# Kernel tuning notes

Hardware: AMD Instinct MI355X
Metric: run time of the kernel (lower is better)

## Reference

```python
import jax, jax.numpy as jnp
import numpy as np

N = 10000       # nodes
E = 640000      # edges
D_IN = 128
D_OUT = 128
EPS = 1e-5      # LayerNorm eps (torch default)


def setup_inputs() -> dict:
    key = jax.random.key(0)
    k_x, k_e, k_w, k_b, k_g = jax.random.split(key, 5)
    x = jax.random.normal(k_x, (N, D_IN), dtype=jnp.float32)
    edge_index = jax.random.randint(k_e, (2, E), 0, N, dtype=jnp.int64)
    # GCNConv linear weight (PyG uses glorot) and bias
    lim = float(np.sqrt(6.0 / (D_IN + D_OUT)))
    W = jax.random.uniform(k_w, (D_IN, D_OUT), minval=-lim, maxval=lim, dtype=jnp.float32)
    b = jnp.zeros((D_OUT,), dtype=jnp.float32)
    # LayerNorm affine params
    gamma = jnp.ones((D_OUT,), dtype=jnp.float32)
    beta = jnp.zeros((D_OUT,), dtype=jnp.float32)
    return {"x": x, "edge_index": edge_index, "W": W, "b": b, "gamma": gamma, "beta": beta}


def reference(x, edge_index, W, b, gamma, beta):
    # --- GCNConv: A_hat = D^{-1/2} (A + I) D^{-1/2}; out = A_hat X W + b ---
    self_idx = jnp.arange(N, dtype=edge_index.dtype)
    src = jnp.concatenate([edge_index[0], self_idx])  # [E+N]
    dst = jnp.concatenate([edge_index[1], self_idx])  # [E+N]
    deg = jax.ops.segment_sum(jnp.ones_like(src, dtype=x.dtype), dst, num_segments=N)
    dinv = jnp.where(deg > 0, jax.lax.rsqrt(deg), 0.0)  # [N]
    norm = dinv[src] * dinv[dst]                        # [E+N]
    h = x @ W                                           # [N, D_OUT] transform first (cheaper)
    msg = h[src] * norm[:, None]                        # [E+N, D_OUT]
    out = jax.ops.segment_sum(msg, dst, num_segments=N) + b
    # --- LayerNorm over feature dim ---
    mu = jnp.mean(out, axis=-1, keepdims=True)
    var = jnp.mean(jnp.square(out - mu), axis=-1, keepdims=True)
    out = (out - mu) * jax.lax.rsqrt(var + EPS) * gamma + beta
    # act = Identity (last_act=ReLU is truthy -> Identity branch); dropout = eval identity; residual=False
    return out
```

## Files before the change

### kernel.cpp

```cpp
#include <hip/hip_runtime.h>
#include <hip/hip_fp16.h>

#define D 128
#define LN_EPS 1e-5f


static __device__ __forceinline__ float h2f(unsigned short h) {
    return __half2float(__builtin_bit_cast(__half, h));
}
static __device__ __forceinline__ unsigned short f2h(float f) {
    return __builtin_bit_cast(unsigned short, __float2half_rn(f));
}

static __device__ __forceinline__ void flagbar(int* slots, int c, int C, int phase) {
    __syncthreads();
    int val = 0x5A5A0001 + phase;
    int tid = threadIdx.x;
    if (tid == 0)
        __hip_atomic_store(&slots[phase * 64 + c], val, __ATOMIC_RELEASE, __HIP_MEMORY_SCOPE_AGENT);
    if (tid < C) {
        while (__hip_atomic_load(&slots[phase * 64 + tid], __ATOMIC_ACQUIRE, __HIP_MEMORY_SCOPE_AGENT) != val)
            __builtin_amdgcn_s_sleep(1);
    }
    __syncthreads();
}

__global__ __launch_bounds__(1024) void build_kernel(
        const int* __restrict__ src, const int* __restrict__ dst,
        const float* __restrict__ W, unsigned int* __restrict__ Wh,
        unsigned short* __restrict__ ghist, int* __restrict__ blocksum,
        int* __restrict__ rowptr, float* __restrict__ dinv,
        unsigned short* __restrict__ csr, int* __restrict__ bar,
        int N, int E, int Ec, int NW, int C) {
    extern __shared__ int lds[];
    __shared__ int s_scan[20];
    int c = blockIdx.x;
    int tid = threadIdx.x;
    int lane = tid & 63, wv = tid >> 6;

    for (int i = tid; i < N; i += 1024) lds[i] = 0;
    int gs = gridDim.x * 1024;
    for (int i = c * 1024 + tid; i < NW; i += gs) {
        float2 v = ((const float2*)W)[i];
        Wh[i] = (unsigned int)f2h(v.x) | ((unsigned int)f2h(v.y) << 16);
    }
    __syncthreads();
    int lo = c * Ec, hi = min(lo + Ec, E);
    #pragma unroll 4
    for (int i = lo + tid; i < hi; i += 1024)
        atomicAdd(&lds[dst[i]], 1);
    __syncthreads();
    for (int i = tid; i < N; i += 1024)
        ghist[(size_t)c * N + i] = (unsigned short)lds[i];
    flagbar(bar, c, C, 0);

    int nper = (N + C - 1) / C;
    int n0 = c * nper;
    int nn = min(nper, N - n0); if (nn < 0) nn = 0;
    int mydeg = 0;
    if (tid < nn) {
        int n = n0 + tid;
        int run = 0;
        #pragma unroll 8
        for (int cc = 0; cc < C; cc++) {
            int t = ghist[(size_t)cc * N + n];
            ghist[(size_t)cc * N + n] = (unsigned short)run;
            run += t;
        }
        mydeg = run;
        dinv[n] = rsqrtf((float)(run + 1));
    }
    int incl = mydeg;
    #pragma unroll
    for (int off = 1; off < 64; off <<= 1) {
        int y = __shfl_up(incl, off);
        if (lane >= off) incl += y;
    }
    if (lane == 63) s_scan[wv] = incl;
    __syncthreads();
    if (tid == 0) {
        int run = 0;
        #pragma unroll
        for (int k = 0; k < 16; k++) { int t = s_scan[k]; s_scan[k] = run; run += t; }
        blocksum[c] = run;
    }
    __syncthreads();
    if (tid < nn) rowptr[n0 + tid] = s_scan[wv] + incl - mydeg;
    flagbar(bar, c, C, 1);

    if (tid < 64) {
        int bs = (tid < C) ? blocksum[tid] : 0;
        int inc2 = bs;
        #pragma unroll
        for (int off = 1; off < 64; off <<= 1) {
            int y = __shfl_up(inc2, off);
            if (tid >= off) inc2 += y;
        }
        if (tid == c)     s_scan[18] = inc2 - bs;
        if (tid == C - 1) s_scan[19] = inc2;
    }
    __syncthreads();
    int base = s_scan[18];
    if (tid < nn) rowptr[n0 + tid] += base;
    if (c == C - 1 && tid == 0) rowptr[N] = s_scan[19];
    flagbar(bar, c, C, 2);

    for (int i = tid; i < N; i += 1024)
        lds[i] = rowptr[i] + ghist[(size_t)c * N + i];
    __syncthreads();
    #pragma unroll 4
    for (int i = lo + tid; i < hi; i += 1024) {
        int d = dst[i];
        int pos = atomicAdd(&lds[d], 1);
        csr[pos] = (unsigned short)src[i];
    }
}

__global__ __launch_bounds__(1024) void gemm_half(const float* __restrict__ x,
                                                  const unsigned int* __restrict__ Wh,
                                                  const float* __restrict__ dinv,
                                                  unsigned int* __restrict__ Hh,
                                                  int N) {
    int wv = threadIdx.x >> 6, lane = threadIdx.x & 63;
    int gw = blockIdx.x * 16 + wv;
    int totw = gridDim.x * 16;
    for (int r = gw; r < N; r += totw) {
        float2 xr = ((const float2*)x)[r * 64 + lane];
        float y0 = 0.f, y1 = 0.f;
        #pragma unroll 8
        for (int k = 0; k < 64; k++) {
            float g0 = __shfl(xr.x, k);
            float g1 = __shfl(xr.y, k);
            unsigned int w0 = Wh[(2 * k) * 64 + lane];
            unsigned int w1 = Wh[(2 * k + 1) * 64 + lane];
            y0 += g0 * h2f((unsigned short)w0) + g1 * h2f((unsigned short)w1);
            y1 += g0 * h2f((unsigned short)(w0 >> 16)) + g1 * h2f((unsigned short)(w1 >> 16));
        }
        float dr = dinv[r];
        Hh[r * 64 + lane] = (unsigned int)f2h(y0 * dr) | ((unsigned int)f2h(y1 * dr) << 16);
    }
}

__global__ __launch_bounds__(512) void fused_agg(const unsigned int* __restrict__ Hh,
                                                 const int* __restrict__ rowptr,
                                                 const unsigned short* __restrict__ csr,
                                                 const float* __restrict__ dinv,
                                                 const float* __restrict__ bias,
                                                 const float* __restrict__ gamma,
                                                 const float* __restrict__ beta,
                                                 float* __restrict__ out, int N) {
    int w = threadIdx.x >> 6, lane = threadIdx.x & 63;
    int node = blockIdx.x * 8 + w;
    if (node >= N) return;
    float dn = dinv[node];

    unsigned int hv0 = Hh[node * 64 + lane];
    float a0 = h2f((unsigned short)hv0);
    float a1 = h2f((unsigned short)(hv0 >> 16));

    int start = rowptr[node], end = rowptr[node + 1];
    int base = start;
    for (; base + 64 <= end; base += 64) {
        int s = csr[base + lane];
        #pragma unroll 8
        for (int k = 0; k < 64; k++) {
            int sk = __shfl(s, k);
            unsigned int hv = Hh[sk * 64 + lane];
            a0 += h2f((unsigned short)hv);
            a1 += h2f((unsigned short)(hv >> 16));
        }
    }
    int rem = end - base;
    if (rem > 0) {
        int s = 0;
        if (lane < rem) s = csr[base + lane];
        for (int k = 0; k < rem; k++) {
            int sk = __shfl(s, k);
            unsigned int hv = Hh[sk * 64 + lane];
            a0 += h2f((unsigned short)hv);
            a1 += h2f((unsigned short)(hv >> 16));
        }
    }

    int c0 = lane * 2;
    float y0 = dn * a0 + bias[c0];
    float y1 = dn * a1 + bias[c0 + 1];

    float sum = y0 + y1, sq = y0 * y0 + y1 * y1;
    #pragma unroll
    for (int off = 32; off > 0; off >>= 1) {
        sum += __shfl_xor(sum, off);
        sq  += __shfl_xor(sq, off);
    }
    float mean = sum * (1.0f / D);
    float var  = sq * (1.0f / D) - mean * mean;
    float inv  = rsqrtf(var + LN_EPS);
    float o0 = (y0 - mean) * inv * gamma[c0] + beta[c0];
    float o1 = (y1 - mean) * inv * gamma[c0 + 1] + beta[c0 + 1];
    *(float2*)(out + (size_t)node * D + c0) = make_float2(o0, o1);
}


__global__ void deg_kernel(const int* __restrict__ dst, int* __restrict__ deg, int E) {
    int e = blockIdx.x * blockDim.x + threadIdx.x;
    if (e < E) atomicAdd(&deg[dst[e]], 1);
}
__global__ __launch_bounds__(1024) void scan_kernel(const int* __restrict__ deg,
                                                    int* __restrict__ rowptr,
                                                    int* __restrict__ fill,
                                                    float* __restrict__ dinv, int N) {
    __shared__ int s_wsum[16];
    __shared__ int s_woff[16];
    __shared__ int s_carry;
    int t = threadIdx.x;
    int lane = t & 63, w = t >> 6;
    if (t == 0) s_carry = 0;
    __syncthreads();
    for (int base = 0; base < N; base += 1024) {
        int i = base + t;
        int v = (i < N) ? deg[i] : 0;
        int incl = v;
        #pragma unroll
        for (int off = 1; off < 64; off <<= 1) {
            int y = __shfl_up(incl, off);
            if (lane >= off) incl += y;
        }
        if (lane == 63) s_wsum[w] = incl;
        __syncthreads();
        if (t == 0) {
            int run = s_carry;
            #pragma unroll
            for (int k = 0; k < 16; k++) { s_woff[k] = run; run += s_wsum[k]; }
            s_carry = run;
        }
        __syncthreads();
        if (i < N) {
            int rp = s_woff[w] + (incl - v);
            rowptr[i] = rp;
            fill[i] = rp;
            dinv[i] = rsqrtf((float)(v + 1));
        }
    }
    if (t == 0) rowptr[N] = s_carry;
}
__global__ void fill_kernel(const int* __restrict__ src, const int* __restrict__ dst,
                            int* __restrict__ fill, unsigned short* __restrict__ csr, int E) {
    int e = blockIdx.x * blockDim.x + threadIdx.x;
    if (e < E) {
        int pos = atomicAdd(&fill[dst[e]], 1);
        csr[pos] = (unsigned short)src[e];
    }
}
__global__ __launch_bounds__(512) void fused_fp32(const float* __restrict__ x,
                                                  const float* __restrict__ W,
                                                  const int* __restrict__ rowptr,
                                                  const unsigned short* __restrict__ csr,
                                                  const float* __restrict__ dinv,
                                                  const float* __restrict__ bias,
                                                  const float* __restrict__ gamma,
                                                  const float* __restrict__ beta,
                                                  float* __restrict__ out, int N) {
    __shared__ float sW[D * D];
    {
        const float4* Wv = (const float4*)W;
        float4* sWv = (float4*)sW;
        #pragma unroll
        for (int i = 0; i < (D * D / 4) / 512; i++)
            sWv[threadIdx.x + i * 512] = Wv[threadIdx.x + i * 512];
    }
    __syncthreads();
    int w = threadIdx.x >> 6, lane = threadIdx.x & 63;
    int node = blockIdx.x * 8 + w;
    if (node >= N) return;
    float dn = dinv[node];
    int c0 = lane * 2;
    float2 xv = *(const float2*)(x + (size_t)node * D + c0);
    float a0 = xv.x * dn * dn, a1 = xv.y * dn * dn;
    int start = rowptr[node], end = rowptr[node + 1];
    int base = start;
    for (; base + 64 <= end; base += 64) {
        int s = csr[base + lane];
        float wt = dinv[s] * dn;
        #pragma unroll 8
        for (int k = 0; k < 64; k++) {
            int sk = __shfl(s, k);
            float wk = __shfl(wt, k);
            float2 xs = *(const float2*)(x + (size_t)sk * D + c0);
            a0 += xs.x * wk; a1 += xs.y * wk;
        }
    }
    int rem = end - base;
    if (rem > 0) {
        int s = 0; float wt = 0.f;
        if (lane < rem) { s = csr[base + lane]; wt = dinv[s] * dn; }
        for (int k = 0; k < rem; k++) {
            int sk = __shfl(s, k);
            float wk = __shfl(wt, k);
            float2 xs = *(const float2*)(x + (size_t)sk * D + c0);
            a0 += xs.x * wk; a1 += xs.y * wk;
        }
    }
    float y0 = bias[c0], y1 = bias[c0 + 1];
    #pragma unroll 8
    for (int k = 0; k < 64; k++) {
        float g0 = __shfl(a0, k);
        float g1 = __shfl(a1, k);
        float2 w0 = *(const float2*)(sW + (2 * k) * D + c0);
        float2 w1 = *(const float2*)(sW + (2 * k + 1) * D + c0);
        y0 += g0 * w0.x + g1 * w1.x;
        y1 += g0 * w0.y + g1 * w1.y;
    }
    float sum = y0 + y1, sq = y0 * y0 + y1 * y1;
    #pragma unroll
    for (int off = 32; off > 0; off >>= 1) {
        sum += __shfl_xor(sum, off);
        sq  += __shfl_xor(sq, off);
    }
    float mean = sum * (1.0f / D);
    float var  = sq * (1.0f / D) - mean * mean;
    float inv  = rsqrtf(var + LN_EPS);
    float o0 = (y0 - mean) * inv * gamma[c0] + beta[c0];
    float o1 = (y1 - mean) * inv * gamma[c0 + 1] + beta[c0 + 1];
    *(float2*)(out + (size_t)node * D + c0) = make_float2(o0, o1);
}

extern "C" void kernel_launch(void* const* d_in, const int* in_sizes, int n_in,
                              void* d_out, int out_size, void* d_ws, size_t ws_size,
                              hipStream_t stream) {
    const float* x     = (const float*)d_in[0];
    const int*   ei    = (const int*)d_in[1];
    const float* W     = (const float*)d_in[2];
    const float* bias  = (const float*)d_in[3];
    const float* gamma = (const float*)d_in[4];
    const float* beta  = (const float*)d_in[5];
    float*       out   = (float*)d_out;

    int N = in_sizes[0] / D;
    int E = in_sizes[1] / 2;
    const int* src = ei;
    const int* dst = ei + E;

    char* ws = (char*)d_ws;
    size_t off = 0;
    auto carve = [&](size_t bytes) { size_t p = off; off = (off + bytes + 15) & ~15UL; return (void*)(ws + p); };
    int*            bar      = (int*)           carve(3 * 64 * 4);
    int*            blocksum = (int*)           carve(64 * 4);
    int*            rowptr   = (int*)           carve((size_t)(N + 1) * 4);
    float*          dinv     = (float*)         carve((size_t)N * 4);
    unsigned short* csr      = (unsigned short*)carve((size_t)E * 2);
    unsigned int*   Hh       = (unsigned int*)  carve((size_t)N * (D / 2) * 4);
    unsigned int*   Wh       = (unsigned int*)  carve((size_t)D * (D / 2) * 4);
    size_t fixed_end = off;

    int C = 0;
    if (ws_size > fixed_end + 16) {
        size_t avail = ws_size - fixed_end - 16;
        size_t cmax = avail / ((size_t)N * 2);
        C = (int)((cmax > 64) ? 64 : cmax);
    }

    if (C >= 16 && N <= 65535) {
        unsigned short* ghist = (unsigned short*)carve((size_t)C * N * 2);
        int Ec = (E + C - 1) / C;
        int NW = D * (D / 2);
        size_t lds = (size_t)N * 4;
        build_kernel<<<C, 1024, lds, stream>>>(src, dst, W, Wh, ghist,
                                               blocksum, rowptr, dinv, csr, bar,
                                               N, E, Ec, NW, C);
        gemm_half<<<256, 1024, 0, stream>>>(x, Wh, dinv, Hh, N);
        fused_agg<<<(N + 7) / 8, 512, 0, stream>>>(Hh, rowptr, csr, dinv,
                                                   bias, gamma, beta, out, N);
    } else {
        int* deg  = (int*)carve((size_t)N * 4);
        int* fill = (int*)carve((size_t)N * 4);
        hipMemsetAsync(deg, 0, (size_t)N * 4, stream);
        deg_kernel<<<(E + 255) / 256, 256, 0, stream>>>(dst, deg, E);
        scan_kernel<<<1, 1024, 0, stream>>>(deg, rowptr, fill, dinv, N);
        fill_kernel<<<(E + 255) / 256, 256, 0, stream>>>(src, dst, fill, csr, E);
        fused_fp32<<<(N + 7) / 8, 512, 0, stream>>>(x, W, rowptr, csr, dinv,
                                                    bias, gamma, beta, out, N);
    }
}
```

Measured before the change: 153.5 us.

## Fuse half-precision X·W transform into the CSR build kernel

Result: slower. 203.8 us (+32.8%).

```diff
diff --git a/kernel.cpp b/kernel.cpp
--- a/kernel.cpp
+++ b/kernel.cpp
@@ -25,38 +25,65 @@
     __syncthreads();
 }
 
+#define MAXROWS 10
+
 __global__ __launch_bounds__(1024) void build_kernel(
         const int* __restrict__ src, const int* __restrict__ dst,
-        const float* __restrict__ W, unsigned int* __restrict__ Wh,
+        const float* __restrict__ x, const float* __restrict__ W,
+        unsigned int* __restrict__ Hh,
         unsigned short* __restrict__ ghist, int* __restrict__ blocksum,
         int* __restrict__ rowptr, float* __restrict__ dinv,
         unsigned short* __restrict__ csr, int* __restrict__ bar,
-        int N, int E, int Ec, int NW, int C) {
+        int N, int E, int Ec, int C) {
     extern __shared__ int lds[];
+    __shared__ unsigned int s_Wh[D * D / 2];
     __shared__ int s_scan[20];
     int c = blockIdx.x;
     int tid = threadIdx.x;
     int lane = tid & 63, wv = tid >> 6;
 
+    int nper = (N + C - 1) / C;
+    int n0 = c * nper;
+    int nn = min(nper, N - n0); if (nn < 0) nn = 0;
+
     for (int i = tid; i < N; i += 1024) lds[i] = 0;
-    int gs = gridDim.x * 1024;
-    for (int i = c * 1024 + tid; i < NW; i += gs) {
+    #pragma unroll
+    for (int i = tid; i < D * D / 2; i += 1024) {
         float2 v = ((const float2*)W)[i];
-        Wh[i] = (unsigned int)f2h(v.x) | ((unsigned int)f2h(v.y) << 16);
-    }
-    __syncthreads();
+        s_Wh[i] = (unsigned int)f2h(v.x) | ((unsigned int)f2h(v.y) << 16);
+    }
+    __syncthreads();
+
     int lo = c * Ec, hi = min(lo + Ec, E);
     #pragma unroll 4
     for (int i = lo + tid; i < hi; i += 1024)
         atomicAdd(&lds[dst[i]], 1);
+
+    float2 acc[MAXROWS];
+    #pragma unroll
+    for (int j = 0; j < MAXROWS; j++) {
+        acc[j] = make_float2(0.f, 0.f);
+        int r = n0 + wv + 16 * j;
+        if (wv + 16 * j < nn) {
+            float2 xr = ((const float2*)x)[r * 64 + lane];
+            float y0 = 0.f, y1 = 0.f;
+            #pragma unroll 8
+            for (int k = 0; k < 64; k++) {
+                float g0 = __shfl(xr.x, k);
+                float g1 = __shfl(xr.y, k);
+                unsigned int w0 = s_Wh[(2 * k) * 64 + lane];
+                unsigned int w1 = s_Wh[(2 * k + 1) * 64 + lane];
+                y0 += g0 * h2f((unsigned short)w0) + g1 * h2f((unsigned short)w1);
+                y1 += g0 * h2f((unsigned short)(w0 >> 16)) + g1 * h2f((unsigned short)(w1 >> 16));
+            }
+            acc[j] = make_float2(y0, y1);
+        }
+    }
     __syncthreads();
     for (int i = tid; i < N; i += 1024)
         ghist[(size_t)c * N + i] = (unsigned short)lds[i];
     flagbar(bar, c, C, 0);
 
-    int nper = (N + C - 1) / C;
-    int n0 = c * nper;
-    int nn = min(nper, N - n0); if (nn < 0) nn = 0;
     int mydeg = 0;
     if (tid < nn) {
         int n = n0 + tid;
@@ -68,7 +95,9 @@
             run += t;
         }
         mydeg = run;
-        dinv[n] = rsqrtf((float)(run + 1));
+        float dv = rsqrtf((float)(run + 1));
+        dinv[n] = dv;
+        ((float*)lds)[tid] = dv;
     }
     int incl = mydeg;
     #pragma unroll
@@ -99,6 +128,15 @@
         if (tid == c)     s_scan[18] = inc2 - bs;
         if (tid == C - 1) s_scan[19] = inc2;
     }
+    #pragma unroll
+    for (int j = 0; j < MAXROWS; j++) {
+        int lr = wv + 16 * j;
+        if (lr < nn) {
+            float dr = ((float*)lds)[lr];
+            Hh[(size_t)(n0 + lr) * 64 + lane] =
+                (unsigned int)f2h(acc[j].x * dr) | ((unsigned int)f2h(acc[j].y * dr) << 16);
+        }
+    }
     __syncthreads();
     int base = s_scan[18];
     if (tid < nn) rowptr[n0 + tid] += base;
@@ -113,31 +151,6 @@
         int d = dst[i];
         int pos = atomicAdd(&lds[d], 1);
         csr[pos] = (unsigned short)src[i];
-    }
-}
-
-__global__ __launch_bounds__(1024) void gemm_half(const float* __restrict__ x,
-                                                  const unsigned int* __restrict__ Wh,
-                                                  const float* __restrict__ dinv,
-                                                  unsigned int* __restrict__ Hh,
-                                                  int N) {
-    int wv = threadIdx.x >> 6, lane = threadIdx.x & 63;
-    int gw = blockIdx.x * 16 + wv;
-    int totw = gridDim.x * 16;
-    for (int r = gw; r < N; r += totw) {
-        float2 xr = ((const float2*)x)[r * 64 + lane];
-        float y0 = 0.f, y1 = 0.f;
-        #pragma unroll 8
-        for (int k = 0; k < 64; k++) {
-            float g0 = __shfl(xr.x, k);
-            float g1 = __shfl(xr.y, k);
-            unsigned int w0 = Wh[(2 * k) * 64 + lane];
-            unsigned int w1 = Wh[(2 * k + 1) * 64 + lane];
-            y0 += g0 * h2f((unsigned short)w0) + g1 * h2f((unsigned short)w1);
-            y1 += g0 * h2f((unsigned short)(w0 >> 16)) + g1 * h2f((unsigned short)(w1 >> 16));
-        }
-        float dr = dinv[r];
-        Hh[r * 64 + lane] = (unsigned int)f2h(y0 * dr) | ((unsigned int)f2h(y1 * dr) << 16);
     }
 }
 
@@ -349,7 +362,6 @@
     float*          dinv     = (float*)         carve((size_t)N * 4);
     unsigned short* csr      = (unsigned short*)carve((size_t)E * 2);
     unsigned int*   Hh       = (unsigned int*)  carve((size_t)N * (D / 2) * 4);
-    unsigned int*   Wh       = (unsigned int*)  carve((size_t)D * (D / 2) * 4);
     size_t fixed_end = off;
 
     int C = 0;
@@ -359,15 +371,13 @@
         C = (int)((cmax > 64) ? 64 : cmax);
     }
 
-    if (C >= 16 && N <= 65535) {
+    if (C >= 16 && N <= 64 * 16 * MAXROWS) {
         unsigned short* ghist = (unsigned short*)carve((size_t)C * N * 2);
         int Ec = (E + C - 1) / C;
-        int NW = D * (D / 2);
         size_t lds = (size_t)N * 4;
-        build_kernel<<<C, 1024, lds, stream>>>(src, dst, W, Wh, ghist,
+        build_kernel<<<C, 1024, lds, stream>>>(src, dst, x, W, Hh, ghist,
                                                blocksum, rowptr, dinv, csr, bar,
-                                               N, E, Ec, NW, C);
-        gemm_half<<<256, 1024, 0, stream>>>(x, Wh, dinv, Hh, N);
+                                               N, E, Ec, C);
         fused_agg<<<(N + 7) / 8, 512, 0, stream>>>(Hh, rowptr, csr, dinv,
                                                    bias, gamma, beta, out, N);
     } else {
```
